# Kernel optimization log

Hardware: AMD Instinct MI355X
Metric: run time of the kernel (lower is better)

The kernel has to match this reference:

```python
import jax, jax.numpy as jnp
import numpy as np

N, E = 50000, 600000
IN, H, C = 128, 8, 32
HC = H * C
LAT, OUT, NCOM = 32, 64, 30
BN_EPS = 1e-5
NEG_SLOPE = 0.2


def setup_inputs() -> dict:
    key = jax.random.key(0)
    ks = jax.random.split(key, 32)
    f32 = jnp.float32
    def rn(i, shape, s=0.05):
        return jax.random.normal(ks[i], shape, f32) * s
    inp = {
        'x': jax.random.normal(ks[0], (N, IN), f32),
        'eps': jax.random.normal(ks[1], (N, LAT), f32),
        'edge_index': jax.random.randint(ks[2], (2, E), 0, N, jnp.int32),
        # GAT layer 1 (in -> H*C)
        'gat1_W': rn(3, (IN, HC)), 'gat1_asrc': rn(4, (H, C)), 'gat1_adst': rn(5, (H, C)), 'gat1_b': jnp.zeros((HC,), f32),
        'bn1_g': jnp.ones((HC,), f32), 'bn1_b': jnp.zeros((HC,), f32),
        # GAT layer 2 (H*C -> H*C)
        'gat2_W': rn(6, (HC, HC)), 'gat2_asrc': rn(7, (H, C)), 'gat2_adst': rn(8, (H, C)), 'gat2_b': jnp.zeros((HC,), f32),
        'bn2_g': jnp.ones((HC,), f32), 'bn2_b': jnp.zeros((HC,), f32),
        # GAT layer 3 (H*C -> H*C)
        'gat3_W': rn(9, (HC, HC)), 'gat3_asrc': rn(10, (H, C)), 'gat3_adst': rn(11, (H, C)), 'gat3_b': jnp.zeros((HC,), f32),
        'bn3_g': jnp.ones((HC,), f32), 'bn3_b': jnp.zeros((HC,), f32),
        # heads
        'res_W': rn(12, (IN, HC)), 'res_b': jnp.zeros((HC,), f32),
        'mu_W': rn(13, (HC, LAT)), 'mu_b': jnp.zeros((LAT,), f32),
        'lv_W': rn(14, (HC, LAT)), 'lv_b': jnp.zeros((LAT,), f32),
        'dec_W': rn(15, (LAT, OUT)), 'dec_b': jnp.zeros((OUT,), f32),
        'aux_W': rn(16, (HC, NCOM)), 'aux_b': jnp.zeros((NCOM,), f32),
    }
    return inp


def gat_conv(x, src, dst, W, asrc, adst, b):
    # PyG GATConv (concat=True, self-loops already in src/dst, lin bias=False)
    n = x.shape[0]
    h = (x @ W).reshape(n, H, C)                      # [N,H,C]
    a_s = jnp.einsum('nhc,hc->nh', h, asrc)           # [N,H]
    a_d = jnp.einsum('nhc,hc->nh', h, adst)
    e = jax.nn.leaky_relu(a_s[src] + a_d[dst], NEG_SLOPE)  # [E,H]
    m = jax.ops.segment_max(e, dst, num_segments=n)        # per-dest softmax (stable)
    p = jnp.exp(e - m[dst])
    s = jax.ops.segment_sum(p, dst, num_segments=n)
    alpha = p / (s[dst] + 1e-16)                      # [E,H]
    out = jax.ops.segment_sum(h[src] * alpha[:, :, None], dst, num_segments=n)
    return out.reshape(n, HC) + b


def batch_norm(x, g, b):
    mu = x.mean(0)
    var = x.var(0)  # biased var, as torch BN uses for normalization
    return (x - mu) * jax.lax.rsqrt(var + BN_EPS) * g + b


def reference(x, eps, edge_index,
              gat1_W, gat1_asrc, gat1_adst, gat1_b, bn1_g, bn1_b,
              gat2_W, gat2_asrc, gat2_adst, gat2_b, bn2_g, bn2_b,
              gat3_W, gat3_asrc, gat3_adst, gat3_b, bn3_g, bn3_b,
              res_W, res_b, mu_W, mu_b, lv_W, lv_b, dec_W, dec_b, aux_W, aux_b):
    loops = jnp.arange(N, dtype=edge_index.dtype)
    src = jnp.concatenate([edge_index[0], loops])
    dst = jnp.concatenate([edge_index[1], loops])

    residual = x @ res_W + res_b
    h = jax.nn.relu(batch_norm(gat_conv(x, src, dst, gat1_W, gat1_asrc, gat1_adst, gat1_b), bn1_g, bn1_b))
    h = jax.nn.relu(batch_norm(gat_conv(h, src, dst, gat2_W, gat2_asrc, gat2_adst, gat2_b), bn2_g, bn2_b))
    h = jax.nn.relu(batch_norm(gat_conv(h, src, dst, gat3_W, gat3_asrc, gat3_adst, gat3_b), bn3_g, bn3_b))
    h = h + residual

    mu = h @ mu_W + mu_b
    logvar = h @ lv_W + lv_b
    z = mu + eps * jnp.exp(0.5 * logvar)   # reparameterize
    out = z @ dec_W + dec_b
    aux = h @ aux_W + aux_b
    return (out, mu, logvar, aux)
```

## Files before the change

kernel.cpp:

```cpp
#include <hip/hip_runtime.h>

#define N_NODES 50000
#define N_EDGES 600000
#define HC 256
#define NH 8
#define AGG_BLOCKS 2048
#define AGG_WAVES (AGG_BLOCKS * 4)

typedef short s8v __attribute__((ext_vector_type(8)));
typedef float f4v __attribute__((ext_vector_type(4)));
typedef _Float16 h4v __attribute__((ext_vector_type(4)));
typedef __attribute__((address_space(1))) const unsigned int as1_cu32;
typedef __attribute__((address_space(3))) unsigned int as3_u32;

__device__ inline ushort f2bf(float f) {
  unsigned u = __float_as_uint(f);
  unsigned r = u + 0x7FFF + ((u >> 16) & 1);
  return (ushort)(r >> 16);
}

__global__ void k_init_cnt(int* __restrict__ cnt) {
  int i = blockIdx.x * 256 + threadIdx.x;
  if (i < N_NODES) cnt[i] = 1;
}

__global__ void k_count(const int* __restrict__ dstE, int* __restrict__ cnt) {
  int e = blockIdx.x * 256 + threadIdx.x;
  if (e < N_EDGES) atomicAdd(&cnt[dstE[e]], 1);
}

__global__ void k_scan_bsum(const int* __restrict__ cnt, int* __restrict__ bsum) {
  __shared__ int sd[256];
  int i = blockIdx.x * 256 + threadIdx.x;
  sd[threadIdx.x] = (i < N_NODES) ? cnt[i] : 0;
  __syncthreads();
  for (int o = 128; o > 0; o >>= 1) {
    if (threadIdx.x < o) sd[threadIdx.x] += sd[threadIdx.x + o];
    __syncthreads();
  }
  if (threadIdx.x == 0) bsum[blockIdx.x] = sd[0];
}

__global__ void k_scan_offsets(int* __restrict__ bsum, int nb) {
  __shared__ int s[256];
  int t = threadIdx.x;
  int v = (t < nb) ? bsum[t] : 0;
  s[t] = v; __syncthreads();
  for (int o = 1; o < 256; o <<= 1) {
    int x = (t >= o) ? s[t - o] : 0;
    __syncthreads();
    s[t] += x;
    __syncthreads();
  }
  if (t < nb) bsum[t] = s[t] - v;
}

__global__ void k_scan_write(const int* __restrict__ cnt, const int* __restrict__ bsum,
                             int* __restrict__ rowptr, int* __restrict__ fillptr) {
  __shared__ int s[256];
  int t = threadIdx.x;
  int i = blockIdx.x * 256 + t;
  int v = (i < N_NODES) ? cnt[i] : 0;
  s[t] = v; __syncthreads();
  for (int o = 1; o < 256; o <<= 1) {
    int x = (t >= o) ? s[t - o] : 0;
    __syncthreads();
    s[t] += x;
    __syncthreads();
  }
  int excl = s[t] - v + bsum[blockIdx.x];
  if (i < N_NODES) {
    rowptr[i] = excl;
    fillptr[i] = excl;
    if (i == N_NODES - 1) rowptr[N_NODES] = excl + v;
  }
}

__global__ void k_fill(const int* __restrict__ srcE, const int* __restrict__ dstE,
                       int* __restrict__ fillptr, int* __restrict__ srcs) {
  int i = blockIdx.x * 256 + threadIdx.x;
  if (i < N_NODES) {
    int pos = atomicAdd(&fillptr[i], 1);
    srcs[pos] = i;
  } else if (i < N_NODES + N_EDGES) {
    int e = i - N_NODES;
    int pos = atomicAdd(&fillptr[dstE[e]], 1);
    srcs[pos] = srcE[e];
  }
}

__global__ void k_cvt_x(const float* __restrict__ X, ushort* __restrict__ Xb) {
  size_t i = ((size_t)blockIdx.x * 256 + threadIdx.x) * 4;
  float4 x4 = *(const float4*)&X[i];
  ushort4 o;
  o.x = f2bf(x4.x); o.y = f2bf(x4.y); o.z = f2bf(x4.z); o.w = f2bf(x4.w);
  *(ushort4*)&Xb[i] = o;
}

__global__ void k_cvt_wt(const float* __restrict__ W, ushort* __restrict__ Wt, int K, int Nw) {
  __shared__ ushort s[32][33];
  int tx = threadIdx.x & 31, ty = threadIdx.x >> 5;
  int k0 = blockIdx.x * 32, n0 = blockIdx.y * 32;
  for (int j = 0; j < 32; j += 8)
    s[ty + j][tx] = f2bf(W[(size_t)(k0 + ty + j) * Nw + n0 + tx]);
  __syncthreads();
  for (int j = 0; j < 32; j += 8)
    Wt[(size_t)(n0 + ty + j) * K + k0 + tx] = s[tx][ty + j];
}

__global__ void k_pack_head(const float* __restrict__ muW, const float* __restrict__ lvW,
                            const float* __restrict__ auxW, ushort* __restrict__ Wth) {
  int n = blockIdx.x;
  int k = threadIdx.x;
  float v = 0.f;
  if (n < 32) v = muW[k * 32 + n];
  else if (n < 64) v = lvW[k * 32 + (n - 32)];
  else if (n < 94) v = auxW[k * 30 + (n - 64)];
  Wth[n * 256 + k] = f2bf(v);
}

template <typename OutT>
__launch_bounds__(256)
__global__ void k_gemm_bf16(const ushort* __restrict__ A, const ushort* __restrict__ Wt,
                            const float* __restrict__ bias, OutT* __restrict__ Out,
                            int M, int K, int ldc) {
  __shared__ __align__(16) ushort As[16 * 512];
  __shared__ __align__(16) ushort Bs[16 * 512];
  int t = threadIdx.x, w = t >> 6, L = t & 63;
  int bm = blockIdx.x * 128, bn = blockIdx.y * 128;
  int lrow = L & 15, lcol = (L >> 4) * 8;

  const ushort* ga[4];
  const ushort* gb[4];
#pragma unroll
  for (int u = 0; u < 4; u++) {
    int i = w * 4 + u;
    int mt = i >> 1, ks = i & 1;
    int arow = bm + mt * 16 + lrow;
    if (arow >= M) arow = M - 1;
    ga[u] = A + (size_t)arow * K + ks * 32 + lcol;
    int brow = bn + mt * 16 + lrow;
    gb[u] = Wt + (size_t)brow * K + ks * 32 + lcol;
  }

  f4v acc[4][4];
  f4v zero = {0.f, 0.f, 0.f, 0.f};
#pragma unroll
  for (int mi = 0; mi < 4; mi++)
#pragma unroll
    for (int ni = 0; ni < 4; ni++) acc[mi][ni] = zero;

  int wm = (w >> 1) * 4;
  int wn = (w & 1) * 4;

  int nk = K >> 6;
  for (int kt = 0; kt < nk; kt++) {
#pragma unroll
    for (int u = 0; u < 4; u++) {
      int i = w * 4 + u;
      __builtin_amdgcn_global_load_lds((as1_cu32*)ga[u], (as3_u32*)&As[i * 512], 16, 0, 0);
      __builtin_amdgcn_global_load_lds((as1_cu32*)gb[u], (as3_u32*)&Bs[i * 512], 16, 0, 0);
      ga[u] += 64; gb[u] += 64;
    }
    __syncthreads();
#pragma unroll
    for (int ks = 0; ks < 2; ks++) {
      s8v af[4], bf[4];
#pragma unroll
      for (int mi = 0; mi < 4; mi++)
        af[mi] = *(const s8v*)&As[(((wm + mi) * 2 + ks) * 64 + L) * 8];
#pragma unroll
      for (int ni = 0; ni < 4; ni++)
        bf[ni] = *(const s8v*)&Bs[(((wn + ni) * 2 + ks) * 64 + L) * 8];
#pragma unroll
      for (int mi = 0; mi < 4; mi++)
#pragma unroll
        for (int ni = 0; ni < 4; ni++)
          acc[mi][ni] = __builtin_amdgcn_mfma_f32_16x16x32_bf16(af[mi], bf[ni], acc[mi][ni], 0, 0, 0);
    }
    __syncthreads();
  }
#pragma unroll
  for (int ni = 0; ni < 4; ni++) {
    int col = bn + (wn + ni) * 16 + (L & 15);
    float bb = bias ? bias[col] : 0.f;
#pragma unroll
    for (int mi = 0; mi < 4; mi++) {
      int rbase = bm + (wm + mi) * 16 + (L >> 4) * 4;
#pragma unroll
      for (int i = 0; i < 4; i++) {
        int r = rbase + i;
        if (r < M) Out[(size_t)r * ldc + col] = (OutT)(acc[mi][ni][i] + bb);
      }
    }
  }
}

__launch_bounds__(256)
__global__ void k_att(const _Float16* __restrict__ B, const float* __restrict__ asrc,
                      const float* __restrict__ adst,
                      float* __restrict__ as_, float* __restrict__ ad_) {
  int wid = (blockIdx.x * 256 + threadIdx.x) >> 6;
  int lane = threadIdx.x & 63;
  h4v x = *(const h4v*)&B[(size_t)wid * 256 + (lane << 2)];
  float4 s4 = *(const float4*)&asrc[lane << 2];
  float4 d4 = *(const float4*)&adst[lane << 2];
  float x0 = (float)x[0], x1 = (float)x[1], x2 = (float)x[2], x3 = (float)x[3];
  float vs = x0 * s4.x + x1 * s4.y + x2 * s4.z + x3 * s4.w;
  float vd = x0 * d4.x + x1 * d4.y + x2 * d4.z + x3 * d4.w;
  vs += __shfl_xor(vs, 1); vs += __shfl_xor(vs, 2); vs += __shfl_xor(vs, 4);
  vd += __shfl_xor(vd, 1); vd += __shfl_xor(vd, 2); vd += __shfl_xor(vd, 4);
  if ((lane & 7) == 0) {
    as_[wid * NH + (lane >> 3)] = vs;
    ad_[wid * NH + (lane >> 3)] = vd;
  }
}

__launch_bounds__(256)
__global__ void k_agg(const int* __restrict__ rowptr, const int* __restrict__ srcs,
                      const float* __restrict__ as_, const float* __restrict__ ad_,
                      const _Float16* __restrict__ B, const float* __restrict__ gb,
                      _Float16* __restrict__ C, float* __restrict__ part,
                      float* __restrict__ stats) {
  __shared__ float ss[4 * 512];
  int t = threadIdx.x;
  if (blockIdx.x == 0) {
    stats[t] = 0.f; stats[t + 256] = 0.f;
  }
  int w = t >> 6, lane = t & 63;
  int h = lane >> 3;
  int cb = lane << 2;
  float4 g4 = *(const float4*)&gb[cb];
  float sts0 = 0.f, sts1 = 0.f, sts2 = 0.f, sts3 = 0.f;
  float stq0 = 0.f, stq1 = 0.f, stq2 = 0.f, stq3 = 0.f;

  for (int n = blockIdx.x * 4 + w; n < N_NODES; n += AGG_WAVES) {
    int beg = rowptr[n], end = rowptr[n + 1];
    float ad_nh = ad_[n * NH + h];
    float ac0 = 0.f, ac1 = 0.f, ac2 = 0.f, ac3 = 0.f, wsum = 0.f;
    int k = beg;
    for (; k + 4 <= end; k += 4) {
      int s0 = srcs[k], s1 = srcs[k + 1], s2 = srcs[k + 2], s3 = srcs[k + 3];
      h4v b0 = *(const h4v*)&B[(size_t)s0 * 256 + cb];
      h4v b1 = *(const h4v*)&B[(size_t)s1 * 256 + cb];
      h4v b2 = *(const h4v*)&B[(size_t)s2 * 256 + cb];
      h4v b3 = *(const h4v*)&B[(size_t)s3 * 256 + cb];
      float e0 = as_[s0 * NH + h] + ad_nh; e0 = e0 > 0.f ? e0 : 0.2f * e0;
      float e1 = as_[s1 * NH + h] + ad_nh; e1 = e1 > 0.f ? e1 : 0.2f * e1;
      float e2 = as_[s2 * NH + h] + ad_nh; e2 = e2 > 0.f ? e2 : 0.2f * e2;
      float e3 = as_[s3 * NH + h] + ad_nh; e3 = e3 > 0.f ? e3 : 0.2f * e3;
      float p0 = __expf(e0), p1 = __expf(e1), p2 = __expf(e2), p3 = __expf(e3);
      wsum += (p0 + p1) + (p2 + p3);
      ac0 += p0 * (float)b0[0] + p1 * (float)b1[0] + p2 * (float)b2[0] + p3 * (float)b3[0];
      ac1 += p0 * (float)b0[1] + p1 * (float)b1[1] + p2 * (float)b2[1] + p3 * (float)b3[1];
      ac2 += p0 * (float)b0[2] + p1 * (float)b1[2] + p2 * (float)b2[2] + p3 * (float)b3[2];
      ac3 += p0 * (float)b0[3] + p1 * (float)b1[3] + p2 * (float)b2[3] + p3 * (float)b3[3];
    }
    for (; k < end; k++) {
      int s = srcs[k];
      h4v b4 = *(const h4v*)&B[(size_t)s * 256 + cb];
      float e = as_[s * NH + h] + ad_nh;
      e = e > 0.f ? e : 0.2f * e;
      float p = __expf(e);
      wsum += p;
      ac0 += p * (float)b4[0]; ac1 += p * (float)b4[1];
      ac2 += p * (float)b4[2]; ac3 += p * (float)b4[3];
    }
    float inv = 1.f / (wsum + 1e-16f);
    float v0 = ac0 * inv + g4.x, v1 = ac1 * inv + g4.y;
    float v2 = ac2 * inv + g4.z, v3 = ac3 * inv + g4.w;
    h4v o; o[0] = (_Float16)v0; o[1] = (_Float16)v1; o[2] = (_Float16)v2; o[3] = (_Float16)v3;
    *(h4v*)&C[(size_t)n * 256 + cb] = o;
    sts0 += v0; stq0 += v0 * v0;
    sts1 += v1; stq1 += v1 * v1;
    sts2 += v2; stq2 += v2 * v2;
    sts3 += v3; stq3 += v3 * v3;
  }
  float* sw = &ss[w * 512];
  sw[cb + 0] = sts0; sw[cb + 1] = sts1; sw[cb + 2] = sts2; sw[cb + 3] = sts3;
  sw[256 + cb + 0] = stq0; sw[256 + cb + 1] = stq1;
  sw[256 + cb + 2] = stq2; sw[256 + cb + 3] = stq3;
  __syncthreads();
  float p0 = ss[t] + ss[512 + t] + ss[1024 + t] + ss[1536 + t];
  float p1 = ss[256 + t] + ss[768 + t] + ss[1280 + t] + ss[1792 + t];
  part[(size_t)blockIdx.x * 512 + t] = p0;
  part[(size_t)blockIdx.x * 512 + 256 + t] = p1;
}

__global__ void k_bn_reduce(const float* __restrict__ part, float* __restrict__ stats) {
  int i = threadIdx.x;
  int base = blockIdx.x * (AGG_BLOCKS / 16);
  float s0 = 0.f, s1 = 0.f;
  for (int b = 0; b < AGG_BLOCKS / 16; b++) {
    s0 += part[(size_t)(base + b) * 512 + i];
    s1 += part[(size_t)(base + b) * 512 + 256 + i];
  }
  atomicAdd(&stats[i], s0);
  atomicAdd(&stats[256 + i], s1);
}

__global__ void k_bn_relu_cvt(const _Float16* __restrict__ X, const float* __restrict__ stats,
                              const float* __restrict__ g, const float* __restrict__ b,
                              const _Float16* __restrict__ resid, ushort* __restrict__ Xb) {
  size_t i = ((size_t)blockIdx.x * 256 + threadIdx.x) * 4;
  int c = (int)(i & 255);
  const float invN = 1.f / (float)N_NODES;
  h4v x4 = *(const h4v*)&X[i];
  float4 s4 = *(const float4*)&stats[c];
  float4 q4 = *(const float4*)&stats[256 + c];
  float4 g4 = *(const float4*)&g[c];
  float4 b4 = *(const float4*)&b[c];
  float m0 = s4.x * invN, m1 = s4.y * invN, m2 = s4.z * invN, m3 = s4.w * invN;
  float v0 = ((float)x4[0] - m0) * rsqrtf(q4.x * invN - m0 * m0 + 1e-5f) * g4.x + b4.x;
  float v1 = ((float)x4[1] - m1) * rsqrtf(q4.y * invN - m1 * m1 + 1e-5f) * g4.y + b4.y;
  float v2 = ((float)x4[2] - m2) * rsqrtf(q4.z * invN - m2 * m2 + 1e-5f) * g4.z + b4.z;
  float v3 = ((float)x4[3] - m3) * rsqrtf(q4.w * invN - m3 * m3 + 1e-5f) * g4.w + b4.w;
  v0 = v0 > 0.f ? v0 : 0.f; v1 = v1 > 0.f ? v1 : 0.f;
  v2 = v2 > 0.f ? v2 : 0.f; v3 = v3 > 0.f ? v3 : 0.f;
  if (resid) {
    h4v r4 = *(const h4v*)&resid[i];
    v0 += (float)r4[0]; v1 += (float)r4[1]; v2 += (float)r4[2]; v3 += (float)r4[3];
  }
  ushort4 ob;
  ob.x = f2bf(v0); ob.y = f2bf(v1); ob.z = f2bf(v2); ob.w = f2bf(v3);
  *(ushort4*)&Xb[i] = ob;
}

__launch_bounds__(256)
__global__ void k_dec(const _Float16* __restrict__ Hd, const float* __restrict__ eps,
                      const float* __restrict__ mub, const float* __restrict__ lvb,
                      const float* __restrict__ auxb,
                      const float* __restrict__ decW, const float* __restrict__ decb,
                      float* __restrict__ out) {
  __shared__ float wsd[2048];
  __shared__ float shz[4][32];
  int t = threadIdx.x;
  for (int i = t; i < 2048; i += 256) wsd[i] = decW[i];
  int w = t >> 6, lane = t & 63;
  int n = blockIdx.x * 4 + w;
  const _Float16* hd = &Hd[(size_t)n * 128];
  if (lane < 32) {
    float mu = (float)hd[lane] + mub[lane];
    float lv = (float)hd[32 + lane] + lvb[lane];
    out[(size_t)N_NODES * 64 + (size_t)n * 32 + lane] = mu;
    out[(size_t)N_NODES * 96 + (size_t)n * 32 + lane] = lv;
    shz[w][lane] = mu + eps[(size_t)n * 32 + lane] * __expf(0.5f * lv);
  } else if (lane < 62) {
    int j = lane - 32;
    out[(size_t)N_NODES * 128 + (size_t)n * 30 + j] = (float)hd[64 + j] + auxb[j];
  }
  __syncthreads();
  float o = decb[lane];
#pragma unroll 8
  for (int k = 0; k < 32; k++) o += shz[w][k] * wsd[k * 64 + lane];
  out[(size_t)n * 64 + lane] = o;
}

extern "C" void kernel_launch(void* const* d_in, const int* in_sizes, int n_in,
                              void* d_out, int out_size, void* d_ws, size_t ws_size,
                              hipStream_t stream) {
  (void)in_sizes; (void)n_in; (void)out_size; (void)ws_size;
  const float* x    = (const float*)d_in[0];
  const float* eps  = (const float*)d_in[1];
  const int*   ei   = (const int*)d_in[2];
  const float* gW[3]    = {(const float*)d_in[3],  (const float*)d_in[9],  (const float*)d_in[15]};
  const float* gasrc[3] = {(const float*)d_in[4],  (const float*)d_in[10], (const float*)d_in[16]};
  const float* gadst[3] = {(const float*)d_in[5],  (const float*)d_in[11], (const float*)d_in[17]};
  const float* gbias[3] = {(const float*)d_in[6],  (const float*)d_in[12], (const float*)d_in[18]};
  const float* bng[3]   = {(const float*)d_in[7],  (const float*)d_in[13], (const float*)d_in[19]};
  const float* bnb[3]   = {(const float*)d_in[8],  (const float*)d_in[14], (const float*)d_in[20]};
  const float* resW = (const float*)d_in[21];
  const float* resb = (const float*)d_in[22];
  const float* muW  = (const float*)d_in[23];
  const float* mub  = (const float*)d_in[24];
  const float* lvW  = (const float*)d_in[25];
  const float* lvb  = (const float*)d_in[26];
  const float* decW = (const float*)d_in[27];
  const float* decb = (const float*)d_in[28];
  const float* auxW = (const float*)d_in[29];
  const float* auxb = (const float*)d_in[30];
  float* out = (float*)d_out;

  char* ws = (char*)d_ws;
  size_t off = 0;
  auto alloc = [&](size_t bytes) -> void* {
    void* p = ws + off;
    off += (bytes + 255) & ~(size_t)255;
    return p;
  };
  _Float16* X0  = (_Float16*)alloc((size_t)N_NODES * HC * 2);
  _Float16* X1  = (_Float16*)alloc((size_t)N_NODES * HC * 2);
  _Float16* Rr  = (_Float16*)alloc((size_t)N_NODES * HC * 2);
  _Float16* Hd  = (_Float16*)alloc((size_t)N_NODES * 128 * 2);
  ushort* Xb    = (ushort*)alloc((size_t)N_NODES * HC * 2);
  float*  as_   = (float*)alloc((size_t)N_NODES * NH * 4);
  float*  ad_   = (float*)alloc((size_t)N_NODES * NH * 4);
  float*  stats = (float*)alloc(512 * 4);
  float*  part  = (float*)alloc((size_t)AGG_BLOCKS * 512 * 4);
  int* cnt      = (int*)alloc((size_t)N_NODES * 4);
  int* rowptr   = (int*)alloc((size_t)(N_NODES + 1) * 4);
  int* fillptr  = (int*)alloc((size_t)N_NODES * 4);
  int* srcs     = (int*)alloc((size_t)(N_NODES + N_EDGES) * 4);
  int* bsum     = (int*)alloc(256 * 4);
  ushort* Wt1   = (ushort*)alloc(256 * 128 * 2);
  ushort* Wt2   = (ushort*)alloc(256 * 256 * 2);
  ushort* Wt3   = (ushort*)alloc(256 * 256 * 2);
  ushort* WtR   = (ushort*)alloc(256 * 128 * 2);
  ushort* Wth   = (ushort*)alloc(128 * 256 * 2);

  const int NB = (N_NODES + 255) / 256;
  k_init_cnt<<<NB, 256, 0, stream>>>(cnt);
  k_count<<<(N_EDGES + 255) / 256, 256, 0, stream>>>(ei + N_EDGES, cnt);
  k_scan_bsum<<<NB, 256, 0, stream>>>(cnt, bsum);
  k_scan_offsets<<<1, 256, 0, stream>>>(bsum, NB);
  k_scan_write<<<NB, 256, 0, stream>>>(cnt, bsum, rowptr, fillptr);
  k_fill<<<(N_NODES + N_EDGES + 255) / 256, 256, 0, stream>>>(ei, ei + N_EDGES, fillptr, srcs);

  k_cvt_wt<<<dim3(4, 8), 256, 0, stream>>>(gW[0], Wt1, 128, 256);
  k_cvt_wt<<<dim3(8, 8), 256, 0, stream>>>(gW[1], Wt2, 256, 256);
  k_cvt_wt<<<dim3(8, 8), 256, 0, stream>>>(gW[2], Wt3, 256, 256);
  k_cvt_wt<<<dim3(4, 8), 256, 0, stream>>>(resW, WtR, 128, 256);
  k_pack_head<<<128, 256, 0, stream>>>(muW, lvW, auxW, Wth);
  k_cvt_x<<<(N_NODES * 128) / 1024, 256, 0, stream>>>(x, Xb);

  const int GM = (N_NODES + 127) / 128;
  k_gemm_bf16<_Float16><<<dim3(GM, 2), 256, 0, stream>>>(Xb, WtR, resb, Rr, N_NODES, 128, 256);

  const ushort* Wts[3] = {Wt1, Wt2, Wt3};
  int K = 128;
  for (int L = 0; L < 3; L++) {
    k_gemm_bf16<_Float16><<<dim3(GM, 2), 256, 0, stream>>>(Xb, Wts[L], nullptr, X0, N_NODES, K, 256);
    k_att<<<N_NODES / 4, 256, 0, stream>>>(X0, gasrc[L], gadst[L], as_, ad_);
    k_agg<<<AGG_BLOCKS, 256, 0, stream>>>(rowptr, srcs, as_, ad_, X0, gbias[L], X1, part, stats);
    k_bn_reduce<<<16, 256, 0, stream>>>(part, stats);
    k_bn_relu_cvt<<<(N_NODES * HC) / 1024, 256, 0, stream>>>(
        X1, stats, bng[L], bnb[L], (L == 2) ? Rr : nullptr, Xb);
    K = 256;
  }
  k_gemm_bf16<_Float16><<<dim3(GM, 1), 256, 0, stream>>>(Xb, Wth, nullptr, Hd, N_NODES, 256, 128);
  k_dec<<<N_NODES / 4, 256, 0, stream>>>(Hd, eps, mub, lvb, auxb, decW, decb, out);
}
```

Baseline: 653.4 us.

## Fuse residual GEMM with layer-1 GEMM, use fma_mix in aggregation, widen BN kernel

Concatenates the layer-1 GAT weights and the residual projection weights into one 512-wide weight matrix, so a single GEMM reads X once and writes both outputs into a strided buffer. Attention, aggregation and the final BN/residual kernel take a leading-dimension argument so they can read this strided layout. The aggregation inner loop now uses inline v_fma_mix_f32 assembly to multiply fp16 features by fp32 weights directly, avoiding separate conversions. The BN/ReLU/convert kernel processes 8 elements per thread instead of 4. The strided 512-wide buffer costs some gather locality in layer-1 aggregation.

Result: no change. 644.9 us (-1.3%).

```diff
diff --git a/kernel.cpp b/kernel.cpp
--- a/kernel.cpp
+++ b/kernel.cpp
@@ -10,6 +10,7 @@
 typedef short s8v __attribute__((ext_vector_type(8)));
 typedef float f4v __attribute__((ext_vector_type(4)));
 typedef _Float16 h4v __attribute__((ext_vector_type(4)));
+typedef _Float16 h8v __attribute__((ext_vector_type(8)));
 typedef __attribute__((address_space(1))) const unsigned int as1_cu32;
 typedef __attribute__((address_space(3))) unsigned int as3_u32;
 
@@ -122,7 +123,7 @@
 template <typename OutT>
 __launch_bounds__(256)
 __global__ void k_gemm_bf16(const ushort* __restrict__ A, const ushort* __restrict__ Wt,
-                            const float* __restrict__ bias, OutT* __restrict__ Out,
+                            const float* __restrict__ bias, int bias_off, OutT* __restrict__ Out,
                             int M, int K, int ldc) {
   __shared__ __align__(16) ushort As[16 * 512];
   __shared__ __align__(16) ushort Bs[16 * 512];
@@ -183,7 +184,7 @@
 #pragma unroll
   for (int ni = 0; ni < 4; ni++) {
     int col = bn + (wn + ni) * 16 + (L & 15);
-    float bb = bias ? bias[col] : 0.f;
+    float bb = (bias && col >= bias_off) ? bias[col - bias_off] : 0.f;
 #pragma unroll
     for (int mi = 0; mi < 4; mi++) {
       int rbase = bm + (wm + mi) * 16 + (L >> 4) * 4;
@@ -197,12 +198,12 @@
 }
 
 __launch_bounds__(256)
-__global__ void k_att(const _Float16* __restrict__ B, const float* __restrict__ asrc,
+__global__ void k_att(const _Float16* __restrict__ B, int ld, const float* __restrict__ asrc,
                       const float* __restrict__ adst,
                       float* __restrict__ as_, float* __restrict__ ad_) {
   int wid = (blockIdx.x * 256 + threadIdx.x) >> 6;
   int lane = threadIdx.x & 63;
-  h4v x = *(const h4v*)&B[(size_t)wid * 256 + (lane << 2)];
+  h4v x = *(const h4v*)&B[(size_t)wid * ld + (lane << 2)];
   float4 s4 = *(const float4*)&asrc[lane << 2];
   float4 d4 = *(const float4*)&adst[lane << 2];
   float x0 = (float)x[0], x1 = (float)x[1], x2 = (float)x[2], x3 = (float)x[3];
@@ -216,10 +217,20 @@
   }
 }
 
+#define FMA4(P, B2)                                                                        \
+  asm("v_fma_mix_f32 %0, %1, %2, %0 op_sel:[0,0,0] op_sel_hi:[0,1,0]"                      \
+      : "+v"(ac0) : "v"(P), "v"((B2).x));                                                  \
+  asm("v_fma_mix_f32 %0, %1, %2, %0 op_sel:[0,1,0] op_sel_hi:[0,1,0]"                      \
+      : "+v"(ac1) : "v"(P), "v"((B2).x));                                                  \
+  asm("v_fma_mix_f32 %0, %1, %2, %0 op_sel:[0,0,0] op_sel_hi:[0,1,0]"                      \
+      : "+v"(ac2) : "v"(P), "v"((B2).y));                                                  \
+  asm("v_fma_mix_f32 %0, %1, %2, %0 op_sel:[0,1,0] op_sel_hi:[0,1,0]"                      \
+      : "+v"(ac3) : "v"(P), "v"((B2).y));
+
 __launch_bounds__(256)
 __global__ void k_agg(const int* __restrict__ rowptr, const int* __restrict__ srcs,
                       const float* __restrict__ as_, const float* __restrict__ ad_,
-                      const _Float16* __restrict__ B, const float* __restrict__ gb,
+                      const _Float16* __restrict__ B, int ld, const float* __restrict__ gb,
                       _Float16* __restrict__ C, float* __restrict__ part,
                       float* __restrict__ stats) {
   __shared__ float ss[4 * 512];
@@ -230,6 +241,8 @@
   int w = t >> 6, lane = t & 63;
   int h = lane >> 3;
   int cb = lane << 2;
+  int ldu = ld >> 2;
+  const uint2* Bu = (const uint2*)B;
   float4 g4 = *(const float4*)&gb[cb];
   float sts0 = 0.f, sts1 = 0.f, sts2 = 0.f, sts3 = 0.f;
   float stq0 = 0.f, stq1 = 0.f, stq2 = 0.f, stq3 = 0.f;
@@ -241,24 +254,24 @@
     int k = beg;
     for (; k + 4 <= end; k += 4) {
       int s0 = srcs[k], s1 = srcs[k + 1], s2 = srcs[k + 2], s3 = srcs[k + 3];
-      h4v b0 = *(const h4v*)&B[(size_t)s0 * 256 + cb];
-      h4v b1 = *(const h4v*)&B[(size_t)s1 * 256 + cb];
-      h4v b2 = *(const h4v*)&B[(size_t)s2 * 256 + cb];
-      h4v b3 = *(const h4v*)&B[(size_t)s3 * 256 + cb];
+      uint2 b0 = Bu[(size_t)s0 * ldu + lane];
+      uint2 b1 = Bu[(size_t)s1 * ldu + lane];
+      uint2 b2 = Bu[(size_t)s2 * ldu + lane];
+      uint2 b3 = Bu[(size_t)s3 * ldu + lane];
       float e0 = as_[s0 * NH + h] + ad_nh; e0 = e0 > 0.f ? e0 : 0.2f * e0;
       float e1 = as_[s1 * NH + h] + ad_nh; e1 = e1 > 0.f ? e1 : 0.2f * e1;
       float e2 = as_[s2 * NH + h] + ad_nh; e2 = e2 > 0.f ? e2 : 0.2f * e2;
       float e3 = as_[s3 * NH + h] + ad_nh; e3 = e3 > 0.f ? e3 : 0.2f * e3;
       float p0 = __expf(e0), p1 = __expf(e1), p2 = __expf(e2), p3 = __expf(e3);
       wsum += (p0 + p1) + (p2 + p3);
-      ac0 += p0 * (float)b0[0] + p1 * (float)b1[0] + p2 * (float)b2[0] + p3 * (float)b3[0];
-      ac1 += p0 * (float)b0[1] + p1 * (float)b1[1] + p2 * (float)b2[1] + p3 * (float)b3[1];
-      ac2 += p0 * (float)b0[2] + p1 * (float)b1[2] + p2 * (float)b2[2] + p3 * (float)b3[2];
-      ac3 += p0 * (float)b0[3] + p1 * (float)b1[3] + p2 * (float)b2[3] + p3 * (float)b3[3];
+      FMA4(p0, b0)
+      FMA4(p1, b1)
+      FMA4(p2, b2)
+      FMA4(p3, b3)
     }
     for (; k < end; k++) {
       int s = srcs[k];
-      h4v b4 = *(const h4v*)&B[(size_t)s * 256 + cb];
+      h4v b4 = *(const h4v*)&B[(size_t)s * ld + cb];
       float e = as_[s * NH + h] + ad_nh;
       e = e > 0.f ? e : 0.2f * e;
       float p = __expf(e);
@@ -301,29 +314,37 @@
 
 __global__ void k_bn_relu_cvt(const _Float16* __restrict__ X, const float* __restrict__ stats,
                               const float* __restrict__ g, const float* __restrict__ b,
-                              const _Float16* __restrict__ resid, ushort* __restrict__ Xb) {
-  size_t i = ((size_t)blockIdx.x * 256 + threadIdx.x) * 4;
+                              const _Float16* __restrict__ resid, int rld,
+                              ushort* __restrict__ Xb) {
+  size_t i = ((size_t)blockIdx.x * 256 + threadIdx.x) * 8;
   int c = (int)(i & 255);
   const float invN = 1.f / (float)N_NODES;
-  h4v x4 = *(const h4v*)&X[i];
-  float4 s4 = *(const float4*)&stats[c];
-  float4 q4 = *(const float4*)&stats[256 + c];
-  float4 g4 = *(const float4*)&g[c];
-  float4 b4 = *(const float4*)&b[c];
-  float m0 = s4.x * invN, m1 = s4.y * invN, m2 = s4.z * invN, m3 = s4.w * invN;
-  float v0 = ((float)x4[0] - m0) * rsqrtf(q4.x * invN - m0 * m0 + 1e-5f) * g4.x + b4.x;
-  float v1 = ((float)x4[1] - m1) * rsqrtf(q4.y * invN - m1 * m1 + 1e-5f) * g4.y + b4.y;
-  float v2 = ((float)x4[2] - m2) * rsqrtf(q4.z * invN - m2 * m2 + 1e-5f) * g4.z + b4.z;
-  float v3 = ((float)x4[3] - m3) * rsqrtf(q4.w * invN - m3 * m3 + 1e-5f) * g4.w + b4.w;
-  v0 = v0 > 0.f ? v0 : 0.f; v1 = v1 > 0.f ? v1 : 0.f;
-  v2 = v2 > 0.f ? v2 : 0.f; v3 = v3 > 0.f ? v3 : 0.f;
+  h8v x8 = *(const h8v*)&X[i];
+  float v[8];
+#pragma unroll
+  for (int q = 0; q < 2; q++) {
+    float4 s4 = *(const float4*)&stats[c + q * 4];
+    float4 q4 = *(const float4*)&stats[256 + c + q * 4];
+    float4 g4 = *(const float4*)&g[c + q * 4];
+    float4 b4 = *(const float4*)&b[c + q * 4];
+    float m0 = s4.x * invN, m1 = s4.y * invN, m2 = s4.z * invN, m3 = s4.w * invN;
+    v[q * 4 + 0] = ((float)x8[q * 4 + 0] - m0) * rsqrtf(q4.x * invN - m0 * m0 + 1e-5f) * g4.x + b4.x;
+    v[q * 4 + 1] = ((float)x8[q * 4 + 1] - m1) * rsqrtf(q4.y * invN - m1 * m1 + 1e-5f) * g4.y + b4.y;
+    v[q * 4 + 2] = ((float)x8[q * 4 + 2] - m2) * rsqrtf(q4.z * invN - m2 * m2 + 1e-5f) * g4.z + b4.z;
+    v[q * 4 + 3] = ((float)x8[q * 4 + 3] - m3) * rsqrtf(q4.w * invN - m3 * m3 + 1e-5f) * g4.w + b4.w;
+  }
+#pragma unroll
+  for (int q = 0; q < 8; q++) v[q] = v[q] > 0.f ? v[q] : 0.f;
   if (resid) {
-    h4v r4 = *(const h4v*)&resid[i];
-    v0 += (float)r4[0]; v1 += (float)r4[1]; v2 += (float)r4[2]; v3 += (float)r4[3];
-  }
-  ushort4 ob;
-  ob.x = f2bf(v0); ob.y = f2bf(v1); ob.z = f2bf(v2); ob.w = f2bf(v3);
-  *(ushort4*)&Xb[i] = ob;
+    size_t row = i >> 8;
+    h8v r8 = *(const h8v*)&resid[row * rld + c];
+#pragma unroll
+    for (int q = 0; q < 8; q++) v[q] += (float)r8[q];
+  }
+  ushort o8[8];
+#pragma unroll
+  for (int q = 0; q < 8; q++) o8[q] = f2bf(v[q]);
+  *(uint4*)&Xb[i] = *(const uint4*)o8;
 }
 
 __launch_bounds__(256)
@@ -388,9 +409,9 @@
     off += (bytes + 255) & ~(size_t)255;
     return p;
   };
+  _Float16* X0R = (_Float16*)alloc((size_t)N_NODES * 512 * 2);
   _Float16* X0  = (_Float16*)alloc((size_t)N_NODES * HC * 2);
   _Float16* X1  = (_Float16*)alloc((size_t)N_NODES * HC * 2);
-  _Float16* Rr  = (_Float16*)alloc((size_t)N_NODES * HC * 2);
   _Float16* Hd  = (_Float16*)alloc((size_t)N_NODES * 128 * 2);
   ushort* Xb    = (ushort*)alloc((size_t)N_NODES * HC * 2);
   float*  as_   = (float*)alloc((size_t)N_NODES * NH * 4);
@@ -402,10 +423,9 @@
   int* fillptr  = (int*)alloc((size_t)N_NODES * 4);
   int* srcs     = (int*)alloc((size_t)(N_NODES + N_EDGES) * 4);
   int* bsum     = (int*)alloc(256 * 4);
-  ushort* Wt1   = (ushort*)alloc(256 * 128 * 2);
+  ushort* WtP   = (ushort*)alloc(512 * 128 * 2);
   ushort* Wt2   = (ushort*)alloc(256 * 256 * 2);
   ushort* Wt3   = (ushort*)alloc(256 * 256 * 2);
-  ushort* WtR   = (ushort*)alloc(256 * 128 * 2);
   ushort* Wth   = (ushort*)alloc(128 * 256 * 2);
 
   const int NB = (N_NODES + 255) / 256;
@@ -416,27 +436,31 @@
   k_scan_write<<<NB, 256, 0, stream>>>(cnt, bsum, rowptr, fillptr);
   k_fill<<<(N_NODES + N_EDGES + 255) / 256, 256, 0, stream>>>(ei, ei + N_EDGES, fillptr, srcs);
 
-  k_cvt_wt<<<dim3(4, 8), 256, 0, stream>>>(gW[0], Wt1, 128, 256);
+  k_cvt_wt<<<dim3(4, 8), 256, 0, stream>>>(gW[0], WtP, 128, 256);
+  k_cvt_wt<<<dim3(4, 8), 256, 0, stream>>>(resW, WtP + 256 * 128, 128, 256);
   k_cvt_wt<<<dim3(8, 8), 256, 0, stream>>>(gW[1], Wt2, 256, 256);
   k_cvt_wt<<<dim3(8, 8), 256, 0, stream>>>(gW[2], Wt3, 256, 256);
-  k_cvt_wt<<<dim3(4, 8), 256, 0, stream>>>(resW, WtR, 128, 256);
   k_pack_head<<<128, 256, 0, stream>>>(muW, lvW, auxW, Wth);
   k_cvt_x<<<(N_NODES * 128) / 1024, 256, 0, stream>>>(x, Xb);
 
   const int GM = (N_NODES + 127) / 128;
-  k_gemm_bf16<_Float16><<<dim3(GM, 2), 256, 0, stream>>>(Xb, WtR, resb, Rr, N_NODES, 128, 256);
-
-  const ushort* Wts[3] = {Wt1, Wt2, Wt3};
-  int K = 128;
-  for (int L = 0; L < 3; L++) {
-    k_gemm_bf16<_Float16><<<dim3(GM, 2), 256, 0, stream>>>(Xb, Wts[L], nullptr, X0, N_NODES, K, 256);
-    k_att<<<N_NODES / 4, 256, 0, stream>>>(X0, gasrc[L], gadst[L], as_, ad_);
-    k_agg<<<AGG_BLOCKS, 256, 0, stream>>>(rowptr, srcs, as_, ad_, X0, gbias[L], X1, part, stats);
+  const int EW_GRID = (N_NODES * HC) / 2048;
+
+  k_gemm_bf16<_Float16><<<dim3(GM, 4), 256, 0, stream>>>(Xb, WtP, resb, 256, X0R, N_NODES, 128, 512);
+  k_att<<<N_NODES / 4, 256, 0, stream>>>(X0R, 512, gasrc[0], gadst[0], as_, ad_);
+  k_agg<<<AGG_BLOCKS, 256, 0, stream>>>(rowptr, srcs, as_, ad_, X0R, 512, gbias[0], X1, part, stats);
+  k_bn_reduce<<<16, 256, 0, stream>>>(part, stats);
+  k_bn_relu_cvt<<<EW_GRID, 256, 0, stream>>>(X1, stats, bng[0], bnb[0], nullptr, 0, Xb);
+
+  const ushort* Wts[2] = {Wt2, Wt3};
+  for (int L = 0; L < 2; L++) {
+    k_gemm_bf16<_Float16><<<dim3(GM, 2), 256, 0, stream>>>(Xb, Wts[L], nullptr, 0, X0, N_NODES, 256, 256);
+    k_att<<<N_NODES / 4, 256, 0, stream>>>(X0, 256, gasrc[L + 1], gadst[L + 1], as_, ad_);
+    k_agg<<<AGG_BLOCKS, 256, 0, stream>>>(rowptr, srcs, as_, ad_, X0, 256, gbias[L + 1], X1, part, stats);
     k_bn_reduce<<<16, 256, 0, stream>>>(part, stats);
-    k_bn_relu_cvt<<<(N_NODES * HC) / 1024, 256, 0, stream>>>(
-        X1, stats, bng[L], bnb[L], (L == 2) ? Rr : nullptr, Xb);
-    K = 256;
-  }
-  k_gemm_bf16<_Float16><<<dim3(GM, 1), 256, 0, stream>>>(Xb, Wth, nullptr, Hd, N_NODES, 256, 128);
+    k_bn_relu_cvt<<<EW_GRID, 256, 0, stream>>>(
+        X1, stats, bng[L + 1], bnb[L + 1], (L == 1) ? (X0R + 256) : nullptr, 512, Xb);
+  }
+  k_gemm_bf16<_Float16><<<dim3(GM, 1), 256, 0, stream>>>(Xb, Wth, nullptr, 0, Hd, N_NODES, 256, 128);
   k_dec<<<N_NODES / 4, 256, 0, stream>>>(Hd, eps, mub, lvb, auxb, decW, decb, out);
 }
```
